# Kernel tuning notes

Hardware: AMD Instinct MI355X
Metric: run time of the kernel (lower is better)

Reference implementation:

```python
import jax, jax.numpy as jnp
import numpy as np

B, S, D = 8, 2048, 1024
H = 4096          # hidden_dim = 4*dim
E = 8             # num_experts
K = 2             # top_k


def setup_inputs() -> dict:
    key = jax.random.key(0)
    ks = jax.random.split(key, 9)
    def init(k, shape, fan_in):
        return jax.random.normal(k, shape, dtype=jnp.float32) * (1.0 / np.sqrt(fan_in))
    return {
        "x":   jax.random.normal(ks[0], (B, S, D), dtype=jnp.float32),
        # gate params
        "Wg1": init(ks[1], (D, D), D),
        "bg1": jnp.zeros((D,), jnp.float32),
        "Wg2": init(ks[2], (D, E), D),
        "bg2": jnp.zeros((E,), jnp.float32),
        # stacked expert params [E, ...]
        "W1":  init(ks[3], (E, D, H), D),
        "b1":  jnp.zeros((E, H), jnp.float32),
        "W2":  init(ks[4], (E, H, D), H),
        "b2":  jnp.zeros((E, D), jnp.float32),
    }


def reference(x, Wg1, bg1, Wg2, bg2, W1, b1, W2, b2):
    # --- TopKGate: sequence-level routing ---
    routing_input = jnp.mean(x, axis=1)                       # [B, D]
    gh = jax.nn.silu(routing_input @ Wg1 + bg1)               # [B, D]
    logits = gh @ Wg2 + bg2                                   # [B, E]
    topk_logits, topk_idx = jax.lax.top_k(logits, K)          # [B, K]
    topk_w = jax.nn.softmax(topk_logits, axis=-1)             # [B, K]

    # --- Dispatch: gather selected experts' weights per (batch, k) ---
    W1g = W1[topk_idx]                                        # [B, K, D, H]
    b1g = b1[topk_idx]                                        # [B, K, H]
    W2g = W2[topk_idx]                                        # [B, K, H, D]
    b2g = b2[topk_idx]                                        # [B, K, D]

    h = jax.nn.silu(jnp.einsum('bsd,bkdh->bksh', x, W1g) + b1g[:, :, None, :])
    expert_out = jnp.einsum('bksh,bkhd->bksd', h, W2g) + b2g[:, :, None, :]

    # --- Weighted combine ---
    output = jnp.einsum('bk,bksd->bsd', topk_w, expert_out)   # [B, S, D]
    return output, (topk_w, topk_idx)
```

## Files before the change

### kernel.cpp

```cpp
#include <hip/hip_runtime.h>
#include <hip/hip_bf16.h>
#include <cstdint>
#include <cstddef>

typedef unsigned short u16;
typedef __attribute__((ext_vector_type(8))) __bf16 bf16x8;
typedef __attribute__((ext_vector_type(4))) float floatx4;

#define B_ 8
#define S_ 2048
#define D_ 1024
#define H_ 4096
#define E_ 8

__device__ __forceinline__ u16 f2bf(float f) {
    union { float f; unsigned u; } c; c.f = f;
    return (u16)((c.u + 0x7fffu + ((c.u >> 16) & 1u)) >> 16);
}

__device__ __forceinline__ void gload16(const void* g, void* l) {
    __builtin_amdgcn_global_load_lds((__attribute__((address_space(1))) void*)(g),
                                     (__attribute__((address_space(3))) void*)(l),
                                     16, 0, 0);
}

__device__ __forceinline__ void stage(const u16* gbase, int ld, u16* lds, int tid) {
    int wid = tid >> 6;
#pragma unroll
    for (int q = 0; q < 4; ++q) {
        int j = q * 256 + tid;
        int r = j >> 3;
        int c = (j & 7) ^ (r & 7);
        gload16(gbase + (size_t)r * ld + c * 8,
                lds + (size_t)(q * 256 + wid * 64) * 8);
    }
}

__device__ __forceinline__ void stageF(const float* gbase, int ld, u16* lds, int tid) {
#pragma unroll
    for (int q = 0; q < 4; ++q) {
        int j = q * 256 + tid;
        int r = j >> 3;
        int c = (j & 7) ^ (r & 7);
        const float* src = gbase + (size_t)r * ld + c * 8;
        u16 tmp[8];
#pragma unroll
        for (int i = 0; i < 8; ++i) tmp[i] = f2bf(src[i]);
        *(uint4*)(lds + (size_t)j * 8) = *(uint4*)tmp;
    }
}

__device__ __forceinline__ void stageKTF(const float* gbase, int ld, u16* lds, int tid) {
#pragma unroll
    for (int q = 0; q < 4; ++q) {
        int g = q * 256 + tid;
        int k = g >> 4;
        int nc = g & 15;
        const float* src = gbase + (size_t)k * ld + nc * 8;
        int kc = k >> 3, kl = k & 7;
#pragma unroll
        for (int i = 0; i < 8; ++i) {
            int n = nc * 8 + i;
            lds[(((n << 3) + (kc ^ (n & 7))) << 3) + kl] = f2bf(src[i]);
        }
    }
}

__device__ __forceinline__ bf16x8 fragld(const u16* lds, int row, int c) {
    return *(const bf16x8*)(lds + (((row << 3) + (c ^ (row & 7))) << 3));
}

__global__ void mean1_kernel(const float* __restrict__ x, float* __restrict__ part) {
    int d = (blockIdx.x & 3) * 256 + threadIdx.x;
    int b = blockIdx.x >> 2;
    int sc = blockIdx.y;
    const float* p = x + (size_t)b * S_ * D_ + (size_t)sc * 256 * D_ + d;
    float s = 0.f;
#pragma unroll 8
    for (int i = 0; i < 256; ++i) s += p[(size_t)i * D_];
    part[((size_t)b * 8 + sc) * D_ + d] = s;
}

__global__ void mean2_kernel(const float* __restrict__ part, float* __restrict__ ri) {
    int d = (blockIdx.x & 3) * 256 + threadIdx.x;
    int b = blockIdx.x >> 2;
    float s = 0.f;
#pragma unroll
    for (int i = 0; i < 8; ++i) s += part[((size_t)b * 8 + i) * D_ + d];
    ri[b * D_ + d] = s * (1.0f / S_);
}

__global__ void gate1_kernel(const float* __restrict__ ri, const float* __restrict__ Wg1,
                             const float* __restrict__ bg1, float* __restrict__ gh) {
    int j = (blockIdx.x & 3) * 256 + threadIdx.x;
    int b = blockIdx.x >> 2;
    const float* r = ri + b * D_;
    float acc = 0.f;
    for (int i = 0; i < D_; ++i) acc += r[i] * Wg1[(size_t)i * D_ + j];
    acc += bg1[j];
    gh[b * D_ + j] = acc / (1.f + expf(-acc));
}

__global__ void gate2_kernel(const float* __restrict__ gh, const float* __restrict__ Wg2,
                             const float* __restrict__ bg2, float* __restrict__ wgate,
                             int* __restrict__ eidx, float* __restrict__ out) {
    __shared__ float lg[B_ * E_];
    int t = threadIdx.x;
    int b = t >> 3, e = t & 7;
    const float* g = gh + b * D_;
    float acc = 0.f;
    for (int i = 0; i < D_; ++i) acc += g[i] * Wg2[(size_t)i * E_ + e];
    acc += bg2[e];
    lg[t] = acc;
    __syncthreads();
    if (t < B_) {
        float l0 = -1e30f, l1 = -1e30f; int i0 = 0, i1 = 0;
        for (int ee = 0; ee < E_; ++ee) {
            float v = lg[t * E_ + ee];
            if (v > l0) { l1 = l0; i1 = i0; l0 = v; i0 = ee; }
            else if (v > l1) { l1 = v; i1 = ee; }
        }
        float e1 = expf(l1 - l0);
        float w0 = 1.f / (1.f + e1), w1 = e1 / (1.f + e1);
        wgate[t * 2] = w0; wgate[t * 2 + 1] = w1;
        eidx[t * 2] = i0;  eidx[t * 2 + 1] = i1;
        float* ow = out + (size_t)B_ * S_ * D_;
        ow[t * 2] = w0;              ow[t * 2 + 1] = w1;
        ow[16 + t * 2] = (float)i0;  ow[16 + t * 2 + 1] = (float)i1;
    }
}

__global__ void convx_kernel(const float* __restrict__ in, u16* __restrict__ out) {
    size_t i = ((size_t)blockIdx.x * 256 + threadIdx.x) * 8;
    u16 tmp[8];
#pragma unroll
    for (int j = 0; j < 8; ++j) tmp[j] = f2bf(in[i + j]);
    *(uint4*)(out + i) = *(uint4*)tmp;
}

__global__ __launch_bounds__(256) void convT_kernel(const float* __restrict__ in,
                                                    u16* __restrict__ out,
                                                    int R, int C) {
    __shared__ __align__(16) u16 T[64][72];
    int e = blockIdx.z;
    const float* ine = in + (size_t)e * R * C;
    u16* oute = out + (size_t)e * R * C;
    int r0 = blockIdx.y * 64, c0 = blockIdx.x * 64;
    int tid = threadIdx.x;
#pragma unroll
    for (int q = 0; q < 2; ++q) {
        int j = q * 256 + tid;
        int r = j >> 3, ch = j & 7;
        const float* src = ine + (size_t)(r0 + r) * C + c0 + ch * 8;
        u16 tmp[8];
#pragma unroll
        for (int i = 0; i < 8; ++i) tmp[i] = f2bf(src[i]);
        *(uint4*)&T[r][ch * 8] = *(uint4*)tmp;
    }
    __syncthreads();
#pragma unroll
    for (int q = 0; q < 2; ++q) {
        int j = q * 256 + tid;
        int orow = j >> 3, och = j & 7;
        uint4 v; u16* pv = (u16*)&v;
#pragma unroll
        for (int i = 0; i < 8; ++i) pv[i] = T[och * 8 + i][orow];
        *(uint4*)(oute + (size_t)(c0 + orow) * R + r0 + och * 8) = v;
    }
}


#define VMWAIT(N) do { \
    if ((N) == 8) asm volatile("s_waitcnt vmcnt(8)" ::: "memory"); \
    else if ((N) == 4) asm volatile("s_waitcnt vmcnt(4)" ::: "memory"); \
    else if ((N) == 0) asm volatile("s_waitcnt vmcnt(0)" ::: "memory"); \
} while (0)

#define KTILE(kt, STAGEA, STAGEB, VM) do { \
    const u16* sA = lA[(kt) & 3]; const u16* sB = lB[(kt) & 3]; \
    bf16x8 af[4], bfr[4]; \
    _Pragma("unroll") for (int t = 0; t < 4; ++t) af[t] = *(const bf16x8*)(sA + offA[0][t]); \
    _Pragma("unroll") for (int t = 0; t < 4; ++t) bfr[t] = *(const bf16x8*)(sB + offB[t]); \
    STAGEA; \
    __builtin_amdgcn_s_barrier(); \
    asm volatile("s_waitcnt lgkmcnt(0)" ::: "memory"); \
    __builtin_amdgcn_sched_barrier(0); \
    __builtin_amdgcn_s_setprio(1); \
    _Pragma("unroll") for (int mt = 0; mt < 4; ++mt) \
        _Pragma("unroll") for (int nt = 0; nt < 4; ++nt) \
            acc[mt][nt] = __builtin_amdgcn_mfma_f32_16x16x32_bf16(af[mt], bfr[nt], acc[mt][nt], 0, 0, 0); \
    __builtin_amdgcn_s_setprio(0); \
    __builtin_amdgcn_s_barrier(); \
    _Pragma("unroll") for (int t = 0; t < 4; ++t) af[t] = *(const bf16x8*)(sA + offA[1][t]); \
    STAGEB; \
    __builtin_amdgcn_s_barrier(); \
    asm volatile("s_waitcnt lgkmcnt(0)" ::: "memory"); \
    __builtin_amdgcn_sched_barrier(0); \
    __builtin_amdgcn_s_setprio(1); \
    _Pragma("unroll") for (int mt = 0; mt < 4; ++mt) \
        _Pragma("unroll") for (int nt = 0; nt < 4; ++nt) \
            acc[4 + mt][nt] = __builtin_amdgcn_mfma_f32_16x16x32_bf16(af[mt], bfr[nt], acc[4 + mt][nt], 0, 0, 0); \
    __builtin_amdgcn_s_setprio(0); \
    VMWAIT(VM); \
    __builtin_amdgcn_s_barrier(); \
} while (0)

#define SETUP_8P(LDBYTES) \
    const int tid = threadIdx.x, lane = tid & 63, wid = tid >> 6; \
    const int wr = wid >> 2, wc = wid & 3, lr = lane & 15, quad = lane >> 4; \
    int soff[2]; \
    _Pragma("unroll") for (int h = 0; h < 2; ++h) { \
        int g = h * 512 + tid; \
        int r = g >> 2, c = (g & 3) ^ ((g >> 3) & 3); \
        soff[h] = r * (LDBYTES) + c * 16; \
    } \
    const int ldst = wid * 64 * 8; \
    int offA[2][4], offB[4]; \
    _Pragma("unroll") for (int mh = 0; mh < 2; ++mh) \
        _Pragma("unroll") for (int t = 0; t < 4; ++t) { \
            int row = wr * 128 + mh * 64 + t * 16 + lr; \
            offA[mh][t] = (row * 4 + (quad ^ ((row >> 1) & 3))) * 8; \
        } \
    _Pragma("unroll") for (int t = 0; t < 4; ++t) { \
        int row = wc * 64 + t * 16 + lr; \
        offB[t] = (row * 4 + (quad ^ ((row >> 1) & 3))) * 8; \
    } \
    floatx4 acc[8][4] = {};

__global__ __launch_bounds__(512) void gemm1_8p(
    const u16* __restrict__ A, const u16* __restrict__ Bw,
    const float* __restrict__ b1, const int* __restrict__ eidx,
    const float* __restrict__ wgate, u16* __restrict__ hbuf,
    int s0, int hRows) {
    __shared__ __align__(16) u16 lA[4][8192];
    __shared__ __align__(16) u16 lB[4][8192];
    SETUP_8P(D_ * 2)
    const int lp = blockIdx.z, b = lp >> 1;
    const int e = eidx[lp];
    const float wk = wgate[lp];
    const char* Ab = (const char*)(A + (size_t)(b * S_ + s0 + blockIdx.y * 256) * D_);
    const char* Bb = (const char*)(Bw + (size_t)e * H_ * D_ + (size_t)(blockIdx.x * 256) * D_);
    const int NT = D_ / 32;

#define G1_STA(KT3) do { _Pragma("unroll") for (int h = 0; h < 2; ++h) \
        gload16(Ab + soff[h] + (size_t)(KT3) * 64, &lA[(KT3) & 3][h * 4096 + ldst]); } while (0)
#define G1_STB(KT3) do { _Pragma("unroll") for (int h = 0; h < 2; ++h) \
        gload16(Bb + soff[h] + (size_t)(KT3) * 64, &lB[(KT3) & 3][h * 4096 + ldst]); } while (0)

#pragma unroll
    for (int kt = 0; kt < 3; ++kt) { G1_STA(kt); G1_STB(kt); }
    asm volatile("s_waitcnt vmcnt(8)" ::: "memory");
    __builtin_amdgcn_s_barrier();

#pragma unroll 1
    for (int kt = 0; kt < NT - 3; ++kt)
        KTILE(kt, G1_STA(kt + 3), G1_STB(kt + 3), 8);
    KTILE(NT - 3, (void)0, (void)0, 4);
    KTILE(NT - 2, (void)0, (void)0, 0);
    KTILE(NT - 1, (void)0, (void)0, -1);
#undef G1_STA
#undef G1_STB

#pragma unroll
    for (int am = 0; am < 8; ++am)
#pragma unroll
        for (int nt = 0; nt < 4; ++nt) {
            int n = blockIdx.x * 256 + wc * 64 + nt * 16 + lr;
            float bb = b1[e * H_ + n];
#pragma unroll
            for (int r = 0; r < 4; ++r) {
                int mrow = blockIdx.y * 256 + wr * 128 + (am >> 2) * 64 + (am & 3) * 16 + quad * 4 + r;
                float v = acc[am][nt][r] + bb;
                v = v / (1.f + __expf(-v)) * wk;
                hbuf[((size_t)lp * hRows + mrow) * H_ + n] = f2bf(v);
            }
        }
}

__global__ __launch_bounds__(512) void gemm2_8p(
    const u16* __restrict__ hbuf, const u16* __restrict__ Bw,
    const float* __restrict__ b2, const int* __restrict__ eidx,
    const float* __restrict__ wgate, float* __restrict__ out,
    int s0, int hRows) {
    __shared__ __align__(16) u16 lA[4][8192];
    __shared__ __align__(16) u16 lB[4][8192];
    SETUP_8P(H_ * 2)
    const int b = blockIdx.z;
    const int e0 = eidx[b * 2], e1 = eidx[b * 2 + 1];
    const float w0 = wgate[b * 2], w1 = wgate[b * 2 + 1];
    const char* Ab0 = (const char*)(hbuf + ((size_t)(b * 2) * hRows + blockIdx.y * 256) * H_);
    const char* Ab1 = (const char*)(hbuf + ((size_t)(b * 2 + 1) * hRows + blockIdx.y * 256) * H_);
    const char* Bb0 = (const char*)(Bw + (size_t)e0 * D_ * H_ + (size_t)(blockIdx.x * 256) * H_);
    const char* Bb1 = (const char*)(Bw + (size_t)e1 * D_ * H_ + (size_t)(blockIdx.x * 256) * H_);
    const int NT = 2 * H_ / 32;

#define G2_STA(KT3) do { const int kts_ = (KT3); \
        const char* As_ = (kts_ & 128) ? Ab1 : Ab0; \
        _Pragma("unroll") for (int h = 0; h < 2; ++h) \
            gload16(As_ + soff[h] + (size_t)(kts_ & 127) * 64, &lA[kts_ & 3][h * 4096 + ldst]); } while (0)
#define G2_STB(KT3) do { const int kts_ = (KT3); \
        const char* Bs_ = (kts_ & 128) ? Bb1 : Bb0; \
        _Pragma("unroll") for (int h = 0; h < 2; ++h) \
            gload16(Bs_ + soff[h] + (size_t)(kts_ & 127) * 64, &lB[kts_ & 3][h * 4096 + ldst]); } while (0)

#pragma unroll
    for (int kt = 0; kt < 3; ++kt) { G2_STA(kt); G2_STB(kt); }
    asm volatile("s_waitcnt vmcnt(8)" ::: "memory");
    __builtin_amdgcn_s_barrier();

#pragma unroll 1
    for (int kt = 0; kt < NT - 3; ++kt)
        KTILE(kt, G2_STA(kt + 3), G2_STB(kt + 3), 8);
    KTILE(NT - 3, (void)0, (void)0, 4);
    KTILE(NT - 2, (void)0, (void)0, 0);
    KTILE(NT - 1, (void)0, (void)0, -1);
#undef G2_STA
#undef G2_STB

#pragma unroll
    for (int am = 0; am < 8; ++am)
#pragma unroll
        for (int nt = 0; nt < 4; ++nt) {
            int n = blockIdx.x * 256 + wc * 64 + nt * 16 + lr;
            float bb = w0 * b2[e0 * D_ + n] + w1 * b2[e1 * D_ + n];
#pragma unroll
            for (int r = 0; r < 4; ++r) {
                int mrow = blockIdx.y * 256 + wr * 128 + (am >> 2) * 64 + (am & 3) * 16 + quad * 4 + r;
                out[((size_t)b * S_ + s0 + mrow) * D_ + n] = acc[am][nt][r] + bb;
            }
        }
}

template<int BT>
__global__ __launch_bounds__(256) void gemm1_kernel(
    const void* __restrict__ A_, const void* __restrict__ Bw_,
    const float* __restrict__ b1, const int* __restrict__ eidx,
    const float* __restrict__ wgate, u16* __restrict__ hbuf,
    int s0, int hRows, int pbase) {
    __shared__ __align__(16) u16 ldsA[1024 * 8];
    __shared__ __align__(16) u16 ldsB[1024 * 8];
    int tid = threadIdx.x, lane = tid & 63, wid = tid >> 6;
    int wm = wid & 1, wn = wid >> 1, lr = lane & 15, quad = lane >> 4;
    int lp = blockIdx.z, p = pbase + lp, b = p >> 1;
    int e = eidx[p];
    float wk = wgate[p];
    size_t arow = (size_t)(b * S_ + s0 + blockIdx.y * 128);
    floatx4 acc[4][4] = {};
    for (int kk = 0; kk < D_; kk += 64) {
        if (BT == 0) {
            stage((const u16*)A_ + arow * D_ + kk, D_, ldsA, tid);
            stage((const u16*)Bw_ + (size_t)e * H_ * D_ +
                  (size_t)(blockIdx.x * 128) * D_ + kk, D_, ldsB, tid);
        } else {
            stageF((const float*)A_ + arow * D_ + kk, D_, ldsA, tid);
            stageKTF((const float*)Bw_ + (size_t)e * D_ * H_ +
                     (size_t)kk * H_ + blockIdx.x * 128, H_, ldsB, tid);
        }
        __syncthreads();
#pragma unroll
        for (int ks = 0; ks < 2; ++ks) {
            bf16x8 af[4], bfr[4];
#pragma unroll
            for (int t = 0; t < 4; ++t) {
                af[t]  = fragld(ldsA, wm * 64 + t * 16 + lr, ks * 4 + quad);
                bfr[t] = fragld(ldsB, wn * 64 + t * 16 + lr, ks * 4 + quad);
            }
#pragma unroll
            for (int mt = 0; mt < 4; ++mt)
#pragma unroll
                for (int nt = 0; nt < 4; ++nt)
                    acc[mt][nt] = __builtin_amdgcn_mfma_f32_16x16x32_bf16(
                        af[mt], bfr[nt], acc[mt][nt], 0, 0, 0);
        }
        __syncthreads();
    }
#pragma unroll
    for (int mt = 0; mt < 4; ++mt)
#pragma unroll
        for (int nt = 0; nt < 4; ++nt) {
            int n = blockIdx.x * 128 + wn * 64 + nt * 16 + lr;
            float bb = b1[e * H_ + n];
#pragma unroll
            for (int r = 0; r < 4; ++r) {
                int mrow = blockIdx.y * 128 + wm * 64 + mt * 16 + quad * 4 + r;
                float v = acc[mt][nt][r] + bb;
                v = v / (1.f + __expf(-v)) * wk;
                hbuf[((size_t)lp * hRows + mrow) * H_ + n] = f2bf(v);
            }
        }
}

template<int BT>
__global__ __launch_bounds__(256) void gemm2_kernel(
    const u16* __restrict__ hbuf, const void* __restrict__ Bw_,
    const float* __restrict__ b2, const int* __restrict__ eidx,
    const float* __restrict__ wgate, float* __restrict__ out,
    int s0, int hRows, int bbase) {
    __shared__ __align__(16) u16 ldsA[1024 * 8];
    __shared__ __align__(16) u16 ldsB[1024 * 8];
    int tid = threadIdx.x, lane = tid & 63, wid = tid >> 6;
    int wm = wid & 1, wn = wid >> 1, lr = lane & 15, quad = lane >> 4;
    int lb = blockIdx.z, b = bbase + lb;
    floatx4 acc[4][4] = {};
    for (int kp = 0; kp < 2; ++kp) {
        int e = eidx[b * 2 + kp];
        const u16* Abase = hbuf + ((size_t)(lb * 2 + kp) * hRows + blockIdx.y * 128) * H_;
        for (int kk = 0; kk < H_; kk += 64) {
            stage(Abase + kk, H_, ldsA, tid);
            if (BT == 0)
                stage((const u16*)Bw_ + (size_t)e * D_ * H_ +
                      (size_t)(blockIdx.x * 128) * H_ + kk, H_, ldsB, tid);
            else
                stageKTF((const float*)Bw_ + (size_t)e * H_ * D_ +
                         (size_t)kk * D_ + blockIdx.x * 128, D_, ldsB, tid);
            __syncthreads();
#pragma unroll
            for (int ks = 0; ks < 2; ++ks) {
                bf16x8 af[4], bfr[4];
#pragma unroll
                for (int t = 0; t < 4; ++t) {
                    af[t]  = fragld(ldsA, wm * 64 + t * 16 + lr, ks * 4 + quad);
                    bfr[t] = fragld(ldsB, wn * 64 + t * 16 + lr, ks * 4 + quad);
                }
#pragma unroll
                for (int mt = 0; mt < 4; ++mt)
#pragma unroll
                    for (int nt = 0; nt < 4; ++nt)
                        acc[mt][nt] = __builtin_amdgcn_mfma_f32_16x16x32_bf16(
                            af[mt], bfr[nt], acc[mt][nt], 0, 0, 0);
            }
            __syncthreads();
        }
    }
    int e0 = eidx[b * 2], e1 = eidx[b * 2 + 1];
    float w0 = wgate[b * 2], w1 = wgate[b * 2 + 1];
#pragma unroll
    for (int mt = 0; mt < 4; ++mt)
#pragma unroll
        for (int nt = 0; nt < 4; ++nt) {
            int n = blockIdx.x * 128 + wn * 64 + nt * 16 + lr;
            float bb = w0 * b2[e0 * D_ + n] + w1 * b2[e1 * D_ + n];
#pragma unroll
            for (int r = 0; r < 4; ++r) {
                int mrow = blockIdx.y * 128 + wm * 64 + mt * 16 + quad * 4 + r;
                out[((size_t)b * S_ + s0 + mrow) * D_ + n] = acc[mt][nt][r] + bb;
            }
        }
}

extern "C" void kernel_launch(void* const* d_in, const int* in_sizes, int n_in,
                              void* d_out, int out_size, void* d_ws, size_t ws_size,
                              hipStream_t stream) {
    const float* x   = (const float*)d_in[0];
    const float* Wg1 = (const float*)d_in[1];
    const float* bg1 = (const float*)d_in[2];
    const float* Wg2 = (const float*)d_in[3];
    const float* bg2 = (const float*)d_in[4];
    const float* W1  = (const float*)d_in[5];
    const float* b1  = (const float*)d_in[6];
    const float* W2  = (const float*)d_in[7];
    const float* b2  = (const float*)d_in[8];
    float* out = (float*)d_out;
    char* ws = (char*)d_ws;

    float* ri    = (float*)ws;
    float* gh    = (float*)(ws + 32768);
    float* wgate = (float*)(ws + 65536);
    int*   eidx  = (int*)(ws + 65792);
    float* part  = (float*)(ws + 131072);

    const size_t base = (size_t)1 << 20;
    const size_t szXb = (size_t)B_ * S_ * D_ * 2;
    const size_t szW  = (size_t)E_ * D_ * H_ * 2;
    const size_t rowB = (size_t)H_ * 2;

    mean1_kernel<<<dim3(B_ * 4, 8), 256, 0, stream>>>(x, part);
    mean2_kernel<<<dim3(B_ * 4), 256, 0, stream>>>(part, ri);
    gate1_kernel<<<dim3(B_ * 4), 256, 0, stream>>>(ri, Wg1, bg1, gh);
    gate2_kernel<<<1, 64, 0, stream>>>(gh, Wg2, bg2, wgate, eidx, out);

    auto clampSc256 = [](long v) -> int {
        long s = v & ~255L;
        if (s > S_) s = S_;
        if (s < 256) s = 256;
        return (int)s;
    };
    auto clampSc128 = [](long v) -> int {
        long s = v & ~127L;
        if (s > S_) s = S_;
        if (s < 128) s = 128;
        return (int)s;
    };

    if (ws_size >= base + szXb + 2 * szW + (size_t)16 * 256 * rowB) {
        u16* xb   = (u16*)(ws + base);
        u16* W1T  = (u16*)(ws + base + szXb);
        u16* W2T  = (u16*)(ws + base + szXb + szW);
        u16* hbuf = (u16*)(ws + base + szXb + 2 * szW);
        int Sc = clampSc256((long)((ws_size - base - szXb - 2 * szW) / ((size_t)16 * rowB)));
        convx_kernel<<<dim3((B_ * S_ * D_) / (256 * 8)), 256, 0, stream>>>(x, xb);
        convT_kernel<<<dim3(H_ / 64, D_ / 64, E_), 256, 0, stream>>>(W1, W1T, D_, H_);
        convT_kernel<<<dim3(D_ / 64, H_ / 64, E_), 256, 0, stream>>>(W2, W2T, H_, D_);
        for (int s0 = 0; s0 < S_; s0 += Sc) {
            int rows = (S_ - s0 < Sc) ? (S_ - s0) : Sc;
            gemm1_8p<<<dim3(H_ / 256, rows / 256, B_ * 2), 512, 0, stream>>>(
                xb, W1T, b1, eidx, wgate, hbuf, s0, Sc);
            gemm2_8p<<<dim3(D_ / 256, rows / 256, B_), 512, 0, stream>>>(
                hbuf, W2T, b2, eidx, wgate, out, s0, Sc);
        }
    } else {
        u16* hbuf = (u16*)(ws + base);
        long avail = (long)ws_size - (long)base;
        if (avail < 0) avail = 0;
        int Sc = clampSc128(avail / (long)(2 * rowB));
        for (int b = 0; b < B_; ++b) {
            for (int s0 = 0; s0 < S_; s0 += Sc) {
                int rows = (S_ - s0 < Sc) ? (S_ - s0) : Sc;
                gemm1_kernel<1><<<dim3(H_ / 128, rows / 128, 2), 256, 0, stream>>>(
                    x, W1, b1, eidx, wgate, hbuf, s0, Sc, b * 2);
                gemm2_kernel<1><<<dim3(D_ / 128, rows / 128, 1), 256, 0, stream>>>(
                    hbuf, W2, b2, eidx, wgate, out, s0, Sc, b);
            }
        }
    }
}
```

Baseline: 1.204 ms.

## Restructure expert GEMM pipeline to double-buffered K=64 tiles with mid-tile staging

Replaces the 4-stage K=32 LDS ring with a 2-stage ring of K=64 tiles, changing the LDS layout to 8 chunks per row with an XOR swizzle. Each tile loads all B fragments and splits the MFMA work so the next tile's global-to-LDS loads are issued after a barrier partway through compute. It also sets launch bounds of 512 threads with 2 blocks per CU. The goal is fewer barriers per unit of K and better overlap of memory and matrix work. The trade-offs are a shallower prefetch depth, more registers held for fragments, and possible spills under the occupancy hint.

Measured after the change: 2.792 ms. 2.32x slower.

```diff
diff --git a/kernel.cpp b/kernel.cpp
--- a/kernel.cpp
+++ b/kernel.cpp
@@ -22,6 +22,10 @@
     __builtin_amdgcn_global_load_lds((__attribute__((address_space(1))) void*)(g),
                                      (__attribute__((address_space(3))) void*)(l),
                                      16, 0, 0);
+}
+
+__device__ __forceinline__ bf16x8 fragld(const u16* lds, int row, int c) {
+    return *(const bf16x8*)(lds + (((row << 3) + (c ^ (row & 7))) << 3));
 }
 
 __device__ __forceinline__ void stage(const u16* gbase, int ld, u16* lds, int tid) {
@@ -64,10 +68,6 @@
             lds[(((n << 3) + (kc ^ (n & 7))) << 3) + kl] = f2bf(src[i]);
         }
     }
-}
-
-__device__ __forceinline__ bf16x8 fragld(const u16* lds, int row, int c) {
-    return *(const bf16x8*)(lds + (((row << 3) + (c ^ (row & 7))) << 3));
 }
 
 __global__ void mean1_kernel(const float* __restrict__ x, float* __restrict__ part) {
@@ -170,96 +170,84 @@
 }
 
 
-#define VMWAIT(N) do { \
-    if ((N) == 8) asm volatile("s_waitcnt vmcnt(8)" ::: "memory"); \
-    else if ((N) == 4) asm volatile("s_waitcnt vmcnt(4)" ::: "memory"); \
-    else if ((N) == 0) asm volatile("s_waitcnt vmcnt(0)" ::: "memory"); \
-} while (0)
-
-#define KTILE(kt, STAGEA, STAGEB, VM) do { \
-    const u16* sA = lA[(kt) & 3]; const u16* sB = lB[(kt) & 3]; \
-    bf16x8 af[4], bfr[4]; \
-    _Pragma("unroll") for (int t = 0; t < 4; ++t) af[t] = *(const bf16x8*)(sA + offA[0][t]); \
-    _Pragma("unroll") for (int t = 0; t < 4; ++t) bfr[t] = *(const bf16x8*)(sB + offB[t]); \
-    STAGEA; \
-    __builtin_amdgcn_s_barrier(); \
-    asm volatile("s_waitcnt lgkmcnt(0)" ::: "memory"); \
-    __builtin_amdgcn_sched_barrier(0); \
-    __builtin_amdgcn_s_setprio(1); \
+#define VM8  asm volatile("s_waitcnt vmcnt(8)" ::: "memory")
+#define VM0  asm volatile("s_waitcnt vmcnt(0)" ::: "memory")
+#define LG0  asm volatile("s_waitcnt lgkmcnt(0)" ::: "memory")
+
+#define SETUP_V2(LDB) \
+    const int tid = threadIdx.x, lane = tid & 63, wid = tid >> 6; \
+    const int wr = wid >> 2, wc = wid & 3, lr = lane & 15, quad = lane >> 4; \
+    int goff[4], dstg[4]; \
+    _Pragma("unroll") for (int q = 0; q < 4; ++q) { \
+        int j = q * 512 + tid, r = j >> 3, c = (j & 7) ^ (r & 7); \
+        goff[q] = r * (LDB) + c * 16; \
+        dstg[q] = (q * 512 + wid * 64) * 8; \
+    } \
+    floatx4 acc[8][4] = {};
+
+#define TILE_BODY(T, STAGE_STMT, VM_STMT) do { \
+    const u16* sA = lA[(T) & 1]; \
+    const u16* sB = lB[(T) & 1]; \
+    bf16x8 bfv[4][2], a0[4][2], a1[4][2]; \
+    _Pragma("unroll") for (int nt = 0; nt < 4; ++nt) \
+        _Pragma("unroll") for (int ks = 0; ks < 2; ++ks) \
+            bfv[nt][ks] = fragld(sB, wc * 64 + nt * 16 + lr, ks * 4 + quad); \
+    _Pragma("unroll") for (int mt = 0; mt < 4; ++mt) \
+        _Pragma("unroll") for (int ks = 0; ks < 2; ++ks) \
+            a0[mt][ks] = fragld(sA, wr * 128 + mt * 16 + lr, ks * 4 + quad); \
     _Pragma("unroll") for (int mt = 0; mt < 4; ++mt) \
         _Pragma("unroll") for (int nt = 0; nt < 4; ++nt) \
-            acc[mt][nt] = __builtin_amdgcn_mfma_f32_16x16x32_bf16(af[mt], bfr[nt], acc[mt][nt], 0, 0, 0); \
-    __builtin_amdgcn_s_setprio(0); \
-    __builtin_amdgcn_s_barrier(); \
-    _Pragma("unroll") for (int t = 0; t < 4; ++t) af[t] = *(const bf16x8*)(sA + offA[1][t]); \
-    STAGEB; \
-    __builtin_amdgcn_s_barrier(); \
-    asm volatile("s_waitcnt lgkmcnt(0)" ::: "memory"); \
-    __builtin_amdgcn_sched_barrier(0); \
-    __builtin_amdgcn_s_setprio(1); \
+            _Pragma("unroll") for (int ks = 0; ks < 2; ++ks) \
+                acc[mt][nt] = __builtin_amdgcn_mfma_f32_16x16x32_bf16(a0[mt][ks], bfv[nt][ks], acc[mt][nt], 0, 0, 0); \
     _Pragma("unroll") for (int mt = 0; mt < 4; ++mt) \
-        _Pragma("unroll") for (int nt = 0; nt < 4; ++nt) \
-            acc[4 + mt][nt] = __builtin_amdgcn_mfma_f32_16x16x32_bf16(af[mt], bfr[nt], acc[4 + mt][nt], 0, 0, 0); \
-    __builtin_amdgcn_s_setprio(0); \
-    VMWAIT(VM); \
-    __builtin_amdgcn_s_barrier(); \
+        _Pragma("unroll") for (int ks = 0; ks < 2; ++ks) \
+            a1[mt][ks] = fragld(sA, wr * 128 + 64 + mt * 16 + lr, ks * 4 + quad); \
+    _Pragma("unroll") for (int mt = 0; mt < 4; ++mt) \
+        _Pragma("unroll") for (int nt = 0; nt < 2; ++nt) \
+            _Pragma("unroll") for (int ks = 0; ks < 2; ++ks) \
+                acc[4 + mt][nt] = __builtin_amdgcn_mfma_f32_16x16x32_bf16(a1[mt][ks], bfv[nt][ks], acc[4 + mt][nt], 0, 0, 0); \
+    LG0; \
+    __builtin_amdgcn_s_barrier();   \
+    STAGE_STMT; \
+    _Pragma("unroll") for (int mt = 0; mt < 4; ++mt) \
+        _Pragma("unroll") for (int nt = 2; nt < 4; ++nt) \
+            _Pragma("unroll") for (int ks = 0; ks < 2; ++ks) \
+                acc[4 + mt][nt] = __builtin_amdgcn_mfma_f32_16x16x32_bf16(a1[mt][ks], bfv[nt][ks], acc[4 + mt][nt], 0, 0, 0); \
+    VM_STMT; \
+    __builtin_amdgcn_s_barrier();   \
 } while (0)
 
-#define SETUP_8P(LDBYTES) \
-    const int tid = threadIdx.x, lane = tid & 63, wid = tid >> 6; \
-    const int wr = wid >> 2, wc = wid & 3, lr = lane & 15, quad = lane >> 4; \
-    int soff[2]; \
-    _Pragma("unroll") for (int h = 0; h < 2; ++h) { \
-        int g = h * 512 + tid; \
-        int r = g >> 2, c = (g & 3) ^ ((g >> 3) & 3); \
-        soff[h] = r * (LDBYTES) + c * 16; \
-    } \
-    const int ldst = wid * 64 * 8; \
-    int offA[2][4], offB[4]; \
-    _Pragma("unroll") for (int mh = 0; mh < 2; ++mh) \
-        _Pragma("unroll") for (int t = 0; t < 4; ++t) { \
-            int row = wr * 128 + mh * 64 + t * 16 + lr; \
-            offA[mh][t] = (row * 4 + (quad ^ ((row >> 1) & 3))) * 8; \
-        } \
-    _Pragma("unroll") for (int t = 0; t < 4; ++t) { \
-        int row = wc * 64 + t * 16 + lr; \
-        offB[t] = (row * 4 + (quad ^ ((row >> 1) & 3))) * 8; \
-    } \
-    floatx4 acc[8][4] = {};
-
-__global__ __launch_bounds__(512) void gemm1_8p(
+__global__ __launch_bounds__(512, 2) void gemm1_v2(
     const u16* __restrict__ A, const u16* __restrict__ Bw,
     const float* __restrict__ b1, const int* __restrict__ eidx,
     const float* __restrict__ wgate, u16* __restrict__ hbuf,
     int s0, int hRows) {
-    __shared__ __align__(16) u16 lA[4][8192];
-    __shared__ __align__(16) u16 lB[4][8192];
-    SETUP_8P(D_ * 2)
+    __shared__ __align__(16) u16 lA[2][16384];
+    __shared__ __align__(16) u16 lB[2][16384];
+    SETUP_V2(D_ * 2)
     const int lp = blockIdx.z, b = lp >> 1;
     const int e = eidx[lp];
     const float wk = wgate[lp];
     const char* Ab = (const char*)(A + (size_t)(b * S_ + s0 + blockIdx.y * 256) * D_);
     const char* Bb = (const char*)(Bw + (size_t)e * H_ * D_ + (size_t)(blockIdx.x * 256) * D_);
-    const int NT = D_ / 32;
-
-#define G1_STA(KT3) do { _Pragma("unroll") for (int h = 0; h < 2; ++h) \
-        gload16(Ab + soff[h] + (size_t)(KT3) * 64, &lA[(KT3) & 3][h * 4096 + ldst]); } while (0)
-#define G1_STB(KT3) do { _Pragma("unroll") for (int h = 0; h < 2; ++h) \
-        gload16(Bb + soff[h] + (size_t)(KT3) * 64, &lB[(KT3) & 3][h * 4096 + ldst]); } while (0)
-
-#pragma unroll
-    for (int kt = 0; kt < 3; ++kt) { G1_STA(kt); G1_STB(kt); }
-    asm volatile("s_waitcnt vmcnt(8)" ::: "memory");
+    const int NT = D_ / 64;
+
+#define G1_STAGE(T) do { const int kb = (T) * 128, bi = (T) & 1; \
+        _Pragma("unroll") for (int q = 0; q < 4; ++q) gload16(Ab + goff[q] + kb, &lA[bi][dstg[q]]); \
+        _Pragma("unroll") for (int q = 0; q < 4; ++q) gload16(Bb + goff[q] + kb, &lB[bi][dstg[q]]); \
+    } while (0)
+
+    G1_STAGE(0); G1_STAGE(1);
+    VM8;
     __builtin_amdgcn_s_barrier();
 
 #pragma unroll 1
-    for (int kt = 0; kt < NT - 3; ++kt)
-        KTILE(kt, G1_STA(kt + 3), G1_STB(kt + 3), 8);
-    KTILE(NT - 3, (void)0, (void)0, 4);
-    KTILE(NT - 2, (void)0, (void)0, 0);
-    KTILE(NT - 1, (void)0, (void)0, -1);
-#undef G1_STA
-#undef G1_STB
+    for (int t = 0; t < NT; ++t) {
+        if (t + 2 < NT)      TILE_BODY(t, G1_STAGE(t + 2), VM8);
+        else if (t + 1 < NT) TILE_BODY(t, (void)0, VM0);
+        else                 TILE_BODY(t, (void)0, (void)0);
+    }
+#undef G1_STAGE
 
 #pragma unroll
     for (int am = 0; am < 8; ++am)
@@ -277,14 +265,14 @@
         }
 }
 
-__global__ __launch_bounds__(512) void gemm2_8p(
+__global__ __launch_bounds__(512, 2) void gemm2_v2(
     const u16* __restrict__ hbuf, const u16* __restrict__ Bw,
     const float* __restrict__ b2, const int* __restrict__ eidx,
     const float* __restrict__ wgate, float* __restrict__ out,
     int s0, int hRows) {
-    __shared__ __align__(16) u16 lA[4][8192];
-    __shared__ __align__(16) u16 lB[4][8192];
-    SETUP_8P(H_ * 2)
+    __shared__ __align__(16) u16 lA[2][16384];
+    __shared__ __align__(16) u16 lB[2][16384];
+    SETUP_V2(H_ * 2)
     const int b = blockIdx.z;
     const int e0 = eidx[b * 2], e1 = eidx[b * 2 + 1];
     const float w0 = wgate[b * 2], w1 = wgate[b * 2 + 1];
@@ -292,30 +280,26 @@
     const char* Ab1 = (const char*)(hbuf + ((size_t)(b * 2 + 1) * hRows + blockIdx.y * 256) * H_);
     const char* Bb0 = (const char*)(Bw + (size_t)e0 * D_ * H_ + (size_t)(blockIdx.x * 256) * H_);
     const char* Bb1 = (const char*)(Bw + (size_t)e1 * D_ * H_ + (size_t)(blockIdx.x * 256) * H_);
-    const int NT = 2 * H_ / 32;
-
-#define G2_STA(KT3) do { const int kts_ = (KT3); \
-        const char* As_ = (kts_ & 128) ? Ab1 : Ab0; \
-        _Pragma("unroll") for (int h = 0; h < 2; ++h) \
-            gload16(As_ + soff[h] + (size_t)(kts_ & 127) * 64, &lA[kts_ & 3][h * 4096 + ldst]); } while (0)
-#define G2_STB(KT3) do { const int kts_ = (KT3); \
-        const char* Bs_ = (kts_ & 128) ? Bb1 : Bb0; \
-        _Pragma("unroll") for (int h = 0; h < 2; ++h) \
-            gload16(Bs_ + soff[h] + (size_t)(kts_ & 127) * 64, &lB[kts_ & 3][h * 4096 + ldst]); } while (0)
-
-#pragma unroll
-    for (int kt = 0; kt < 3; ++kt) { G2_STA(kt); G2_STB(kt); }
-    asm volatile("s_waitcnt vmcnt(8)" ::: "memory");
+    const int NT = 2 * H_ / 64;
+
+#define G2_STAGE(T) do { const int tt = (T); const int kb = (tt & 63) * 128, bi = tt & 1; \
+        const char* As_ = (tt & 64) ? Ab1 : Ab0; \
+        const char* Bs_ = (tt & 64) ? Bb1 : Bb0; \
+        _Pragma("unroll") for (int q = 0; q < 4; ++q) gload16(As_ + goff[q] + kb, &lA[bi][dstg[q]]); \
+        _Pragma("unroll") for (int q = 0; q < 4; ++q) gload16(Bs_ + goff[q] + kb, &lB[bi][dstg[q]]); \
+    } while (0)
+
+    G2_STAGE(0); G2_STAGE(1);
+    VM8;
     __builtin_amdgcn_s_barrier();
 
 #pragma unroll 1
-    for (int kt = 0; kt < NT - 3; ++kt)
-        KTILE(kt, G2_STA(kt + 3), G2_STB(kt + 3), 8);
-    KTILE(NT - 3, (void)0, (void)0, 4);
-    KTILE(NT - 2, (void)0, (void)0, 0);
-    KTILE(NT - 1, (void)0, (void)0, -1);
-#undef G2_STA
-#undef G2_STB
+    for (int t = 0; t < NT; ++t) {
+        if (t + 2 < NT)      TILE_BODY(t, G2_STAGE(t + 2), VM8);
+        else if (t + 1 < NT) TILE_BODY(t, (void)0, VM0);
+        else                 TILE_BODY(t, (void)0, (void)0);
+    }
+#undef G2_STAGE
 
 #pragma unroll
     for (int am = 0; am < 8; ++am)
@@ -503,9 +487,9 @@
         convT_kernel<<<dim3(D_ / 64, H_ / 64, E_), 256, 0, stream>>>(W2, W2T, H_, D_);
         for (int s0 = 0; s0 < S_; s0 += Sc) {
             int rows = (S_ - s0 < Sc) ? (S_ - s0) : Sc;
-            gemm1_8p<<<dim3(H_ / 256, rows / 256, B_ * 2), 512, 0, stream>>>(
+            gemm1_v2<<<dim3(H_ / 256, rows / 256, B_ * 2), 512, 0, stream>>>(
                 xb, W1T, b1, eidx, wgate, hbuf, s0, Sc);
-            gemm2_8p<<<dim3(D_ / 256, rows / 256, B_), 512, 0, stream>>>(
+            gemm2_v2<<<dim3(D_ / 256, rows / 256, B_), 512, 0, stream>>>(
                 hbuf, W2T, b2, eidx, wgate, out, s0, Sc);
         }
     } else {
```
